# Kernel optimization log

Hardware: AMD Instinct MI355X
Metric: run time of the kernel (lower is better)

The kernel has to match this reference:

```python
import jax, jax.numpy as jnp
import numpy as np

K_TOP = 8
TEMP = 0.1


def setup_inputs() -> dict:
    key = jax.random.key(0)
    k1, k2, k3, k4 = jax.random.split(key, 4)
    B, K, D, Db, C = 256, 64, 256, 512, 1024
    return {
        "slot_features": jax.random.normal(k1, (B, K, D), dtype=jnp.float32),
        "proj_W": jax.random.normal(k2, (D, Db), dtype=jnp.float32) * (1.0 / np.sqrt(D)),
        "proj_b": jax.random.normal(k3, (Db,), dtype=jnp.float32) * 0.01,
        "embed": jax.random.uniform(k4, (C, Db), dtype=jnp.float32),  # NMF atoms are nonnegative
    }


def reference(slot_features, proj_W, proj_b, embed):
    B, K, _ = slot_features.shape
    num_codes = embed.shape[0]

    # slot projection: [B, K, basis_dim]
    z_e = jnp.einsum('bkd,de->bke', slot_features, proj_W) + proj_b
    z_flat = z_e.reshape(B * K, -1)  # [N, Db]

    # Euclidean cdist via expanded squared norm (the GEMM is the heavy part)
    d2 = (jnp.sum(z_flat * z_flat, axis=-1, keepdims=True)
          + jnp.sum(embed * embed, axis=-1)[None, :]
          - 2.0 * (z_flat @ embed.T))  # [N, C]
    dist = jnp.sqrt(jnp.maximum(d2, 0.0))

    # top-k smallest distances
    neg_vals, indices_flat = jax.lax.top_k(-dist, K_TOP)  # [N, k]
    values = -neg_vals
    weights = jax.nn.softmax(-values / TEMP, axis=-1)  # [N, k]

    # gather atoms and interpolate
    selected_atoms = embed[indices_flat]  # [N, k, Db]
    q_flat = jnp.einsum('nk,nkd->nd', weights, selected_atoms)
    q_st = q_flat.reshape(B, K, -1)

    vq_loss = jnp.mean((z_e - jax.lax.stop_gradient(q_st)) ** 2)

    # average usage (equivalent to scatter into [N, C] then mean over N)
    avg_usage = jax.ops.segment_sum(weights.reshape(-1), indices_flat.reshape(-1),
                                    num_segments=num_codes) / (B * K)
    entropy = -jnp.sum(avg_usage * jnp.log(avg_usage + 1e-8))

    indices = indices_flat[:, 0].reshape(B, K)
    return q_st, indices, vq_loss, entropy
```

## Files before the change

### kernel.cpp

```cpp
#include <hip/hip_runtime.h>
#include <math.h>
#include <float.h>

#define NROWS  16384
#define DIN    256
#define DBASIS 512
#define CCODES 1024
#define KTOP   8
#define TEMP_F 0.1f

typedef __attribute__((ext_vector_type(8))) short short8v;
typedef __attribute__((ext_vector_type(4))) float f32x4;

__device__ __forceinline__ unsigned short bf16_rne(float f) {
    unsigned int u = __float_as_uint(f);
    u += 0x7FFFu + ((u >> 16) & 1u);
    return (unsigned short)(u >> 16);
}
__device__ __forceinline__ float bf16_to_f32(unsigned short h) {
    return __uint_as_float(((unsigned int)h) << 16);
}
__device__ __forceinline__ unsigned packkey(float p, float zn2, unsigned cidx) {
    const float d2 = fmaxf(p + zn2, 0.f);
    return (__float_as_uint(d2) & 0xFFFFFC00u) | cidx;
}

#define GLOAD16(gsrc, ldst) \
    __builtin_amdgcn_global_load_lds((const __attribute__((address_space(1))) void*)(gsrc), \
                                     (__attribute__((address_space(3))) void*)(ldst), 16, 0, 0)

__global__ __launch_bounds__(256) void k_prep(const float* __restrict__ embed,
                                              unsigned short* __restrict__ Eh,
                                              unsigned short* __restrict__ El,
                                              float* __restrict__ en2,
                                              float* __restrict__ usage,
                                              float* __restrict__ vq_accum) {
    const int c = blockIdx.x * 256 + threadIdx.x;
    const float4* row = (const float4*)(embed + (size_t)c * DBASIS);
    ushort4* ehr = (ushort4*)(Eh + (size_t)c * DBASIS);
    ushort4* elr = (ushort4*)(El + (size_t)c * DBASIS);
    float s = 0.f;
    #pragma unroll 4
    for (int j = 0; j < DBASIS / 4; ++j) {
        const float4 v = row[j];
        s += v.x * v.x + v.y * v.y + v.z * v.z + v.w * v.w;
        ushort4 h, l;
        h.x = bf16_rne(v.x); l.x = bf16_rne(v.x - bf16_to_f32(h.x));
        h.y = bf16_rne(v.y); l.y = bf16_rne(v.y - bf16_to_f32(h.y));
        h.z = bf16_rne(v.z); l.z = bf16_rne(v.z - bf16_to_f32(h.z));
        h.w = bf16_rne(v.w); l.w = bf16_rne(v.w - bf16_to_f32(h.w));
        ehr[j] = h; elr[j] = l;
    }
    en2[c] = s;
    usage[c] = 0.f;
    if (c == 0) vq_accum[0] = 0.f;
}

__global__ __launch_bounds__(256, 2) void k_gemm_z(const float* __restrict__ A,
                                                   const float* __restrict__ Bm,
                                                   const float* __restrict__ bias,
                                                   float* __restrict__ Z,
                                                   unsigned short* __restrict__ Zh,
                                                   unsigned short* __restrict__ Zl) {
    __shared__ float As[16][132];
    __shared__ float Bs[16][132];
    const int tid = threadIdx.x;
    const int bm = blockIdx.x * 128;
    const int bn = blockIdx.y * 128;
    const int tx = tid & 15, ty = tid >> 4;
    float acc[2][2][4][4] = {};

    for (int k0 = 0; k0 < DIN; k0 += 16) {
        #pragma unroll
        for (int it = 0; it < 2; ++it) {
            const int r  = (tid >> 2) + it * 64;
            const int c4 = (tid & 3) * 4;
            const float4 a = *(const float4*)(A + (size_t)(bm + r) * DIN + k0 + c4);
            As[c4 + 0][r] = a.x; As[c4 + 1][r] = a.y;
            As[c4 + 2][r] = a.z; As[c4 + 3][r] = a.w;
        }
        {
            const int r  = tid >> 4;
            const int c8 = (tid & 15) * 8;
            const float4 b0 = *(const float4*)(Bm + (size_t)(k0 + r) * DBASIS + bn + c8);
            const float4 b1 = *(const float4*)(Bm + (size_t)(k0 + r) * DBASIS + bn + c8 + 4);
            *(float4*)&Bs[r][c8]     = b0;
            *(float4*)&Bs[r][c8 + 4] = b1;
        }
        __syncthreads();
        #pragma unroll
        for (int kk = 0; kk < 16; ++kk) {
            const float4 a0 = *(const float4*)&As[kk][ty * 4];
            const float4 a1 = *(const float4*)&As[kk][64 + ty * 4];
            const float4 b0 = *(const float4*)&Bs[kk][tx * 4];
            const float4 b1 = *(const float4*)&Bs[kk][64 + tx * 4];
            const float av[2][4] = {{a0.x, a0.y, a0.z, a0.w}, {a1.x, a1.y, a1.z, a1.w}};
            const float bv[2][4] = {{b0.x, b0.y, b0.z, b0.w}, {b1.x, b1.y, b1.z, b1.w}};
            #pragma unroll
            for (int qi = 0; qi < 2; ++qi)
                #pragma unroll
                for (int qj = 0; qj < 2; ++qj)
                    #pragma unroll
                    for (int i = 0; i < 4; ++i)
                        #pragma unroll
                        for (int j = 0; j < 4; ++j)
                            acc[qi][qj][i][j] = fmaf(av[qi][i], bv[qj][j], acc[qi][qj][i][j]);
        }
        __syncthreads();
    }
    #pragma unroll
    for (int qj = 0; qj < 2; ++qj) {
        const int colb = bn + qj * 64 + tx * 4;
        const float4 bv = *(const float4*)(bias + colb);
        const float bb[4] = {bv.x, bv.y, bv.z, bv.w};
        #pragma unroll
        for (int qi = 0; qi < 2; ++qi)
            #pragma unroll
            for (int i = 0; i < 4; ++i) {
                const int row = bm + qi * 64 + ty * 4 + i;
                float4 o;
                o.x = acc[qi][qj][i][0] + bb[0];
                o.y = acc[qi][qj][i][1] + bb[1];
                o.z = acc[qi][qj][i][2] + bb[2];
                o.w = acc[qi][qj][i][3] + bb[3];
                *(float4*)(Z + (size_t)row * DBASIS + colb) = o;
                ushort4 h, l;
                h.x = bf16_rne(o.x); l.x = bf16_rne(o.x - bf16_to_f32(h.x));
                h.y = bf16_rne(o.y); l.y = bf16_rne(o.y - bf16_to_f32(h.y));
                h.z = bf16_rne(o.z); l.z = bf16_rne(o.z - bf16_to_f32(h.z));
                h.w = bf16_rne(o.w); l.w = bf16_rne(o.w - bf16_to_f32(h.w));
                *(ushort4*)(Zh + (size_t)row * DBASIS + colb) = h;
                *(ushort4*)(Zl + (size_t)row * DBASIS + colb) = l;
            }
    }
}

__global__ __launch_bounds__(256, 2) void k_gemm_p(const unsigned short* __restrict__ Zh,
                                                   const unsigned short* __restrict__ Zl,
                                                   const unsigned short* __restrict__ Eh,
                                                   const unsigned short* __restrict__ El,
                                                   const float* __restrict__ en2,
                                                   float* __restrict__ P) {
    __shared__ __align__(16) short lds[2][4][4096];
    const int tid  = threadIdx.x;
    const int lane = tid & 63;
    const int w    = tid >> 6;
    const int wr   = w >> 1, wc = w & 1;
    const int bm   = blockIdx.y * 128;
    const int bc   = blockIdx.x * 128;
    const int kg   = lane >> 4;
    const int lr   = lane & 15;

    f32x4 acc[4][4];
    #pragma unroll
    for (int i = 0; i < 4; ++i)
        #pragma unroll
        for (int j = 0; j < 4; ++j)
            acc[i][j] = (f32x4){0.f, 0.f, 0.f, 0.f};

#define STAGE_P(BUF, PH) do {                                                  \
        const int k0_ = (PH) * 32;                                             \
        _Pragma("unroll")                                                      \
        for (int j_ = 0; j_ < 2; ++j_) {                                       \
            const int gi_ = j_ * 256 + tid;                                    \
            const int g_  = gi_ >> 7, r_ = gi_ & 127;                          \
            const size_t ao_ = (size_t)(bm + r_) * DBASIS + k0_ + g_ * 8;      \
            const size_t bo_ = (size_t)(bc + r_) * DBASIS + k0_ + g_ * 8;      \
            GLOAD16(Zh + ao_, &lds[BUF][0][gi_ * 8]);                          \
            GLOAD16(Zl + ao_, &lds[BUF][1][gi_ * 8]);                          \
            GLOAD16(Eh + bo_, &lds[BUF][2][gi_ * 8]);                          \
            GLOAD16(El + bo_, &lds[BUF][3][gi_ * 8]);                          \
        }                                                                      \
    } while (0)

#define COMPUTE_P(BUF) do {                                                    \
        short8v afh[4], afl[4], bfh[4], bfl[4];                                \
        _Pragma("unroll")                                                      \
        for (int f = 0; f < 4; ++f) {                                          \
            const int ai = (kg * 128 + wr * 64 + f * 16 + lr) * 8;             \
            const int bi = (kg * 128 + wc * 64 + f * 16 + lr) * 8;             \
            afh[f] = *(const short8v*)&lds[BUF][0][ai];                        \
            afl[f] = *(const short8v*)&lds[BUF][1][ai];                        \
            bfh[f] = *(const short8v*)&lds[BUF][2][bi];                        \
            bfl[f] = *(const short8v*)&lds[BUF][3][bi];                        \
        }                                                                      \
        _Pragma("unroll")                                                      \
        for (int fm = 0; fm < 4; ++fm)                                         \
            _Pragma("unroll")                                                  \
            for (int fn = 0; fn < 4; ++fn) {                                   \
                acc[fm][fn] = __builtin_amdgcn_mfma_f32_16x16x32_bf16(afh[fm], bfh[fn], acc[fm][fn], 0, 0, 0); \
                acc[fm][fn] = __builtin_amdgcn_mfma_f32_16x16x32_bf16(afh[fm], bfl[fn], acc[fm][fn], 0, 0, 0); \
                acc[fm][fn] = __builtin_amdgcn_mfma_f32_16x16x32_bf16(afl[fm], bfh[fn], acc[fm][fn], 0, 0, 0); \
            }                                                                  \
    } while (0)

    STAGE_P(0, 0);
    __syncthreads();
    int cur = 0;
    for (int ph = 0; ph < 15; ++ph) {
        STAGE_P(cur ^ 1, ph + 1);
        COMPUTE_P(cur);
        __syncthreads();
        cur ^= 1;
    }
    COMPUTE_P(cur);

    #pragma unroll
    for (int fn = 0; fn < 4; ++fn) {
        const int col = bc + wc * 64 + fn * 16 + lr;
        const float e2 = en2[col];
        #pragma unroll
        for (int fm = 0; fm < 4; ++fm) {
            const int row0 = bm + wr * 64 + fm * 16 + (lane >> 4) * 4;
            #pragma unroll
            for (int r = 0; r < 4; ++r)
                P[(size_t)(row0 + r) * CCODES + col] = e2 - 2.f * acc[fm][fn][r];
        }
    }
#undef STAGE_P
#undef COMPUTE_P
}

__global__ __launch_bounds__(256) void k_topk(const float* __restrict__ P,
                                              const float* __restrict__ Z,
                                              const float* __restrict__ embed,
                                              const float* __restrict__ en2,
                                              float* __restrict__ q_out,
                                              float* __restrict__ idx_out,
                                              float* __restrict__ usage,
                                              float* __restrict__ vq_accum) {
    const int tid  = threadIdx.x;
    const int lane = tid & 63;
    const int w    = tid >> 6;
    const int n    = blockIdx.x * 4 + w;

    __shared__ int   cand_lds[4][64];
    __shared__ float ls[4];

    float zv[8];
    float zn2 = 0.f;
    #pragma unroll
    for (int j = 0; j < 8; ++j) {
        zv[j] = Z[(size_t)n * DBASIS + lane + 64 * j];
        zn2 = fmaf(zv[j], zv[j], zn2);
    }
    #pragma unroll
    for (int off = 32; off; off >>= 1) zn2 += __shfl_xor(zn2, off, 64);

    const float4* prow = (const float4*)(P + (size_t)n * CCODES + lane * 16);
    const unsigned cbase = (unsigned)(lane * 16);
    unsigned key[16];
    #pragma unroll
    for (int j = 0; j < 4; ++j) {
        const float4 v = prow[j];
        key[4 * j + 0] = packkey(v.x, zn2, cbase + 4 * j + 0);
        key[4 * j + 1] = packkey(v.y, zn2, cbase + 4 * j + 1);
        key[4 * j + 2] = packkey(v.z, zn2, cbase + 4 * j + 2);
        key[4 * j + 3] = packkey(v.w, zn2, cbase + 4 * j + 3);
    }

    unsigned kmin = key[0];
    #pragma unroll
    for (int t = 1; t < 16; ++t) kmin = (key[t] < kmin) ? key[t] : kmin;

    unsigned lo = 0u, hi = 0xFFFFFFFFu;
    while (lo < hi) {
        const unsigned mid = lo + ((hi - lo) >> 1);
        const unsigned long long mk = __ballot(kmin <= mid);
        if (__popcll(mk) >= 16) hi = mid; else lo = mid + 1;
    }
    const unsigned T = lo;

    int* clist = cand_lds[w];
    int base = 0;
    #pragma unroll
    for (int t = 0; t < 16; ++t) {
        const bool pred = (key[t] <= T);
        const unsigned long long mk = __ballot(pred);
        const int pos = base + __popcll(mk & ((1ull << lane) - 1ull));
        if (pred && pos < 64) clist[pos] = (int)(cbase + t);
        base += __popcll(mk);
    }
    const int m = base < 64 ? base : 64;

    float mydist = FLT_MAX;
    int   myidx  = 0x7FFFFFFF;
    for (int t = 0; t < m; ++t) {
        const int c = clist[t];
        const float* er = embed + (size_t)c * DBASIS;
        float dot = 0.f;
        #pragma unroll
        for (int j = 0; j < 8; ++j) dot = fmaf(zv[j], er[lane + 64 * j], dot);
        #pragma unroll
        for (int off = 32; off; off >>= 1) dot += __shfl_xor(dot, off, 64);
        const float d = sqrtf(fmaxf(zn2 + en2[c] - 2.f * dot, 0.f));
        if (lane == t) { mydist = d; myidx = c; }
    }

    float dist[KTOP];
    int   idx[KTOP];
    #pragma unroll
    for (int p = 0; p < KTOP; ++p) {
        float bv = mydist;
        int   bi = myidx;
        #pragma unroll
        for (int off = 32; off; off >>= 1) {
            const float ov = __shfl_xor(bv, off, 64);
            const int   oi = __shfl_xor(bi, off, 64);
            if (ov < bv || (ov == bv && oi < bi)) { bv = ov; bi = oi; }
        }
        dist[p] = bv; idx[p] = bi;
        if (myidx == bi) { mydist = FLT_MAX; myidx = 0x7FFFFFFF; }
    }

    float wgt[KTOP];
    float s = 0.f;
    #pragma unroll
    for (int t = 0; t < KTOP; ++t) {
        wgt[t] = expf((dist[0] - dist[t]) * (1.0f / TEMP_F));
        s += wgt[t];
    }
    const float inv_s = 1.f / s;
    #pragma unroll
    for (int t = 0; t < KTOP; ++t) wgt[t] *= inv_s;

    float lloss = 0.f;
    #pragma unroll
    for (int j = 0; j < 8; ++j) {
        const int d = lane + 64 * j;
        float acc = 0.f;
        #pragma unroll
        for (int t = 0; t < KTOP; ++t)
            acc = fmaf(wgt[t], embed[(size_t)idx[t] * DBASIS + d], acc);
        q_out[(size_t)n * DBASIS + d] = acc;
        const float df = zv[j] - acc;
        lloss = fmaf(df, df, lloss);
    }
    #pragma unroll
    for (int off = 32; off; off >>= 1) lloss += __shfl_xor(lloss, off, 64);

    if (lane == 0) ls[w] = lloss;
    __syncthreads();
    if (tid == 0) atomicAdd(vq_accum, ls[0] + ls[1] + ls[2] + ls[3]);

    #pragma unroll
    for (int t = 0; t < KTOP; ++t)
        if (lane == t) atomicAdd(usage + idx[t], wgt[t] * (1.0f / (float)NROWS));

    if (lane == 0) idx_out[n] = (float)idx[0];
}

__global__ __launch_bounds__(256) void k_final(const float* __restrict__ usage,
                                               const float* __restrict__ vq_accum,
                                               float* __restrict__ out_scalars) {
    __shared__ float red[256];
    float s = 0.f;
    for (int c = threadIdx.x; c < CCODES; c += 256) {
        const float u = usage[c];
        s += u * logf(u + 1e-8f);
    }
    red[threadIdx.x] = s;
    __syncthreads();
    for (int st = 128; st; st >>= 1) {
        if (threadIdx.x < st) red[threadIdx.x] += red[threadIdx.x + st];
        __syncthreads();
    }
    if (threadIdx.x == 0) {
        out_scalars[0] = vq_accum[0] * (1.0f / ((float)NROWS * (float)DBASIS));
        out_scalars[1] = -red[0];
    }
}

extern "C" void kernel_launch(void* const* d_in, const int* in_sizes, int n_in,
                              void* d_out, int out_size, void* d_ws, size_t ws_size,
                              hipStream_t stream) {
    const float* slot  = (const float*)d_in[0];
    const float* projW = (const float*)d_in[1];
    const float* projb = (const float*)d_in[2];
    const float* embed = (const float*)d_in[3];

    float* out  = (float*)d_out;
    float* q    = out;
    float* idxo = out + (size_t)NROWS * DBASIS;
    float* scal = idxo + NROWS;

    char* wsb = (char*)d_ws;
    float*          Z     = (float*)wsb;          wsb += (size_t)NROWS * DBASIS * 4;
    float*          P     = (float*)wsb;          wsb += (size_t)NROWS * CCODES * 4;
    unsigned short* Zh    = (unsigned short*)wsb; wsb += (size_t)NROWS * DBASIS * 2;
    unsigned short* Zl    = (unsigned short*)wsb; wsb += (size_t)NROWS * DBASIS * 2;
    unsigned short* Eh    = (unsigned short*)wsb; wsb += (size_t)CCODES * DBASIS * 2;
    unsigned short* El    = (unsigned short*)wsb; wsb += (size_t)CCODES * DBASIS * 2;
    float*          en2   = (float*)wsb;          wsb += CCODES * 4;
    float*          usage = (float*)wsb;          wsb += CCODES * 4;
    float*          vq    = (float*)wsb;

    k_prep<<<dim3(CCODES / 256), dim3(256), 0, stream>>>(embed, Eh, El, en2, usage, vq);
    k_gemm_z<<<dim3(NROWS / 128, DBASIS / 128), dim3(256), 0, stream>>>(slot, projW, projb, Z, Zh, Zl);
    k_gemm_p<<<dim3(CCODES / 128, NROWS / 128), dim3(256), 0, stream>>>(Zh, Zl, Eh, El, en2, P);
    k_topk<<<dim3(NROWS / 4), dim3(256), 0, stream>>>(P, Z, embed, en2, q, idxo, usage, vq);
    k_final<<<dim3(1), dim3(256), 0, stream>>>(usage, vq, scal);
}
```

Baseline: 371.9 us.

## Double-buffer projection GEMM and batch candidate rescoring in top-k kernel

```diff
diff --git a/kernel.cpp b/kernel.cpp
--- a/kernel.cpp
+++ b/kernel.cpp
@@ -62,52 +62,81 @@
                                                    float* __restrict__ Z,
                                                    unsigned short* __restrict__ Zh,
                                                    unsigned short* __restrict__ Zl) {
-    __shared__ float As[16][132];
-    __shared__ float Bs[16][132];
+    __shared__ float As[2][16][128];
+    __shared__ float Bs[2][16][128];
     const int tid = threadIdx.x;
     const int bm = blockIdx.x * 128;
     const int bn = blockIdx.y * 128;
     const int tx = tid & 15, ty = tid >> 4;
     float acc[2][2][4][4] = {};
-
-    for (int k0 = 0; k0 < DIN; k0 += 16) {
-        #pragma unroll
-        for (int it = 0; it < 2; ++it) {
-            const int r  = (tid >> 2) + it * 64;
-            const int c4 = (tid & 3) * 4;
-            const float4 a = *(const float4*)(A + (size_t)(bm + r) * DIN + k0 + c4);
-            As[c4 + 0][r] = a.x; As[c4 + 1][r] = a.y;
-            As[c4 + 2][r] = a.z; As[c4 + 3][r] = a.w;
-        }
-        {
-            const int r  = tid >> 4;
-            const int c8 = (tid & 15) * 8;
-            const float4 b0 = *(const float4*)(Bm + (size_t)(k0 + r) * DBASIS + bn + c8);
-            const float4 b1 = *(const float4*)(Bm + (size_t)(k0 + r) * DBASIS + bn + c8 + 4);
-            *(float4*)&Bs[r][c8]     = b0;
-            *(float4*)&Bs[r][c8 + 4] = b1;
-        }
+    float4 a0, a1;
+
+#define LOADA_Z(PH) do {                                                       \
+        const int k0_ = (PH) * 16;                                             \
+        const int r_ = tid >> 2, c4_ = (tid & 3) * 4;                          \
+        a0 = *(const float4*)(A + (size_t)(bm + r_) * DIN + k0_ + c4_);        \
+        a1 = *(const float4*)(A + (size_t)(bm + r_ + 64) * DIN + k0_ + c4_);   \
+    } while (0)
+
+#define WRITEA_Z(BUF) do {                                                     \
+        const int r_ = tid >> 2, c4_ = (tid & 3) * 4;                          \
+        As[BUF][c4_ + 0][r_] = a0.x; As[BUF][c4_ + 1][r_] = a0.y;              \
+        As[BUF][c4_ + 2][r_] = a0.z; As[BUF][c4_ + 3][r_] = a0.w;              \
+        As[BUF][c4_ + 0][r_ + 64] = a1.x; As[BUF][c4_ + 1][r_ + 64] = a1.y;    \
+        As[BUF][c4_ + 2][r_ + 64] = a1.z; As[BUF][c4_ + 3][r_ + 64] = a1.w;    \
+    } while (0)
+
+#define STAGE_B_Z(BUF, PH) do {                                                \
+        const int k0_ = (PH) * 16;                                             \
+        _Pragma("unroll")                                                      \
+        for (int j_ = 0; j_ < 2; ++j_) {                                       \
+            const int gi_ = j_ * 256 + tid;                                    \
+            const int r_ = gi_ >> 5;                                           \
+            const int c4_ = (gi_ & 31) * 4;                                    \
+            GLOAD16(Bm + (size_t)(k0_ + r_) * DBASIS + bn + c4_,               \
+                    &Bs[BUF][r_][c4_]);                                        \
+        }                                                                      \
+    } while (0)
+
+#define COMPUTE_Z(BUF) do {                                                    \
+        _Pragma("unroll")                                                      \
+        for (int kk = 0; kk < 16; ++kk) {                                      \
+            const float4 va0 = *(const float4*)&As[BUF][kk][ty * 4];           \
+            const float4 va1 = *(const float4*)&As[BUF][kk][64 + ty * 4];      \
+            const float4 vb0 = *(const float4*)&Bs[BUF][kk][tx * 4];           \
+            const float4 vb1 = *(const float4*)&Bs[BUF][kk][64 + tx * 4];      \
+            const float av[2][4] = {{va0.x, va0.y, va0.z, va0.w},              \
+                                    {va1.x, va1.y, va1.z, va1.w}};             \
+            const float bv[2][4] = {{vb0.x, vb0.y, vb0.z, vb0.w},              \
+                                    {vb1.x, vb1.y, vb1.z, vb1.w}};             \
+            _Pragma("unroll")                                                  \
+            for (int qi = 0; qi < 2; ++qi)                                     \
+                _Pragma("unroll")                                              \
+                for (int qj = 0; qj < 2; ++qj)                                 \
+                    _Pragma("unroll")                                          \
+                    for (int i = 0; i < 4; ++i)                                \
+                        _Pragma("unroll")                                      \
+                        for (int j = 0; j < 4; ++j)                            \
+                            acc[qi][qj][i][j] =                                \
+                                fmaf(av[qi][i], bv[qj][j], acc[qi][qj][i][j]); \
+        }                                                                      \
+    } while (0)
+
+    LOADA_Z(0);
+    STAGE_B_Z(0, 0);
+    WRITEA_Z(0);
+    __syncthreads();
+    int cur = 0;
+    for (int ph = 0; ph < 15; ++ph) {
+        LOADA_Z(ph + 1);
+        STAGE_B_Z(cur ^ 1, ph + 1);
+        COMPUTE_Z(cur);
+        WRITEA_Z(cur ^ 1);
         __syncthreads();
-        #pragma unroll
-        for (int kk = 0; kk < 16; ++kk) {
-            const float4 a0 = *(const float4*)&As[kk][ty * 4];
-            const float4 a1 = *(const float4*)&As[kk][64 + ty * 4];
-            const float4 b0 = *(const float4*)&Bs[kk][tx * 4];
-            const float4 b1 = *(const float4*)&Bs[kk][64 + tx * 4];
-            const float av[2][4] = {{a0.x, a0.y, a0.z, a0.w}, {a1.x, a1.y, a1.z, a1.w}};
-            const float bv[2][4] = {{b0.x, b0.y, b0.z, b0.w}, {b1.x, b1.y, b1.z, b1.w}};
-            #pragma unroll
-            for (int qi = 0; qi < 2; ++qi)
-                #pragma unroll
-                for (int qj = 0; qj < 2; ++qj)
-                    #pragma unroll
-                    for (int i = 0; i < 4; ++i)
-                        #pragma unroll
-                        for (int j = 0; j < 4; ++j)
-                            acc[qi][qj][i][j] = fmaf(av[qi][i], bv[qj][j], acc[qi][qj][i][j]);
-        }
-        __syncthreads();
-    }
+        cur ^= 1;
+    }
+    COMPUTE_Z(cur);
+
     #pragma unroll
     for (int qj = 0; qj < 2; ++qj) {
         const int colb = bn + qj * 64 + tx * 4;
@@ -133,6 +162,10 @@
                 *(ushort4*)(Zl + (size_t)row * DBASIS + colb) = l;
             }
     }
+#undef LOADA_Z
+#undef WRITEA_Z
+#undef STAGE_B_Z
+#undef COMPUTE_Z
 }
 
 __global__ __launch_bounds__(256, 2) void k_gemm_p(const unsigned short* __restrict__ Zh,
@@ -234,8 +267,9 @@
     const int w    = tid >> 6;
     const int n    = blockIdx.x * 4 + w;
 
-    __shared__ int   cand_lds[4][64];
-    __shared__ float ls[4];
+    __shared__ int      cand_lds[4][64];
+    __shared__ unsigned km_lds[4][64];
+    __shared__ float    ls[4];
 
     float zv[8];
     float zn2 = 0.f;
@@ -263,13 +297,14 @@
     #pragma unroll
     for (int t = 1; t < 16; ++t) kmin = (key[t] < kmin) ? key[t] : kmin;
 
-    unsigned lo = 0u, hi = 0xFFFFFFFFu;
-    while (lo < hi) {
-        const unsigned mid = lo + ((hi - lo) >> 1);
-        const unsigned long long mk = __ballot(kmin <= mid);
-        if (__popcll(mk) >= 16) hi = mid; else lo = mid + 1;
-    }
-    const unsigned T = lo;
+    km_lds[w][lane] = kmin;
+    __syncthreads();
+    int rank = 0;
+    #pragma unroll
+    for (int i = 0; i < 64; ++i) rank += (km_lds[w][i] < kmin) ? 1 : 0;
+    const unsigned long long selm = __ballot(rank == 15);
+    const int src = (int)(__ffsll((long long)selm) - 1);
+    const unsigned T = __shfl(kmin, src, 64);
 
     int* clist = cand_lds[w];
     int base = 0;
@@ -285,16 +320,33 @@
 
     float mydist = FLT_MAX;
     int   myidx  = 0x7FFFFFFF;
-    for (int t = 0; t < m; ++t) {
-        const int c = clist[t];
-        const float* er = embed + (size_t)c * DBASIS;
-        float dot = 0.f;
-        #pragma unroll
-        for (int j = 0; j < 8; ++j) dot = fmaf(zv[j], er[lane + 64 * j], dot);
-        #pragma unroll
-        for (int off = 32; off; off >>= 1) dot += __shfl_xor(dot, off, 64);
-        const float d = sqrtf(fmaxf(zn2 + en2[c] - 2.f * dot, 0.f));
-        if (lane == t) { mydist = d; myidx = c; }
+    for (int t0 = 0; t0 < m; t0 += 4) {
+        int cc[4];
+        #pragma unroll
+        for (int u = 0; u < 4; ++u) {
+            const int tt = t0 + u;
+            cc[u] = clist[tt < m ? tt : (m - 1)];
+        }
+        float dot[4] = {0.f, 0.f, 0.f, 0.f};
+        #pragma unroll
+        for (int j = 0; j < 8; ++j) {
+            const int d = lane + 64 * j;
+            #pragma unroll
+            for (int u = 0; u < 4; ++u)
+                dot[u] = fmaf(zv[j], embed[(size_t)cc[u] * DBASIS + d], dot[u]);
+        }
+        #pragma unroll
+        for (int off = 32; off; off >>= 1) {
+            #pragma unroll
+            for (int u = 0; u < 4; ++u)
+                dot[u] += __shfl_xor(dot[u], off, 64);
+        }
+        #pragma unroll
+        for (int u = 0; u < 4; ++u) {
+            const int tt = t0 + u;
+            const float dd = sqrtf(fmaxf(zn2 + en2[cc[u]] - 2.f * dot[u], 0.f));
+            if (tt < m && lane == tt) { mydist = dd; myidx = cc[u]; }
+        }
     }
 
     float dist[KTOP];
```

Result: faster. 361.7 us (-2.7%).
